# Kernel tuning notes

Hardware: AMD Instinct MI355X
Metric: run time of the kernel (lower is better)

## Reference

```python
import jax, jax.numpy as jnp
import numpy as np


def _segsum(v, idx, n):
    return jax.ops.segment_sum(v, idx, num_segments=n)


def _rdl(z, n_dst, Wna, We, Wi, es, ed, is_, id_):
    """Relationship_Decoupled_layer: node softmax attn + per-edge attn.
    e-channel (mode etype): softmax over 2 logits; i-channel: sigmoid(1 logit)."""
    zd = z[:n_dst]
    node_alpha = jax.nn.softmax(zd @ Wna, axis=1)                      # [nd,2]
    e_e = jax.nn.softmax(jnp.concatenate([z[es], zd[ed]], axis=-1) @ We, axis=1)  # [Ee,2]
    e_i = jax.nn.sigmoid(jnp.concatenate([z[is_], zd[id_]], axis=-1) @ Wi)        # [Ei,1]
    return node_alpha, e_e, e_i


def _one_agg(z, n_dst, W, b, na, e_e, es, ed):
    """One_Neighbor_Aggregation: mean over nbrs of e[:,0]*Linear(z_src), relu, + alpha0*z_dst.
    Linear is applied on src nodes once (linearity) instead of per-edge."""
    zd = na[:, 0:1] * z[:n_dst]
    wz = z @ W + b                                                     # [n_src,D]
    s = _segsum(e_e[:, 0:1] * wz[es], ed, n_dst)                       # [nd,D]
    deg = _segsum(jnp.ones((es.shape[0], 1), z.dtype), ed, n_dst)
    f = jax.nn.relu(s / jnp.maximum(deg, 1.0))
    return f + zd


def _nia(z, n_dst, na, e_e, es, ed, e_i, is_, id_):
    """Neighbor_Interaction_Aggregation: e_h (mode etype, attn col 1) and i_h
    (other etype, sigmoid attn), cross term via polarization identity, + alpha1*z_dst."""
    zd = na[:, 1:2] * z[:n_dst]
    e_h = _segsum(e_e[:, 1:2] * z[es], ed, n_dst)
    i_h = _segsum(e_i * z[is_], id_, n_dst)
    inter = jax.nn.relu(0.5 * (jnp.square(e_h + i_h) - jnp.square(e_h) - jnp.square(i_h)))
    return inter + zd


def setup_inputs() -> dict:
    key = jax.random.key(0)
    ks = jax.random.split(key, 32)
    F, D, O = 256, 128, 64
    n_src0, n_dst0, E0 = 100000, 25000, 500000
    n_src1, n_dst1, E1 = 25000, 5000, 100000

    def ri(k, n, hi):
        return jax.random.randint(k, (n,), 0, hi, dtype=jnp.int32)

    inp = {
        'feat': jax.random.normal(ks[0], (n_src0, F), jnp.float32),
        'src0_cor': ri(ks[1], E0, n_src0), 'dst0_cor': ri(ks[2], E0, n_dst0),
        'src0_sim': ri(ks[3], E0, n_src0), 'dst0_sim': ri(ks[4], E0, n_dst0),
        'src1_cor': ri(ks[5], E1, n_src1), 'dst1_cor': ri(ks[6], E1, n_dst1),
        'src1_sim': ri(ks[7], E1, n_src1), 'dst1_sim': ri(ks[8], E1, n_dst1),
        'n_dst0': n_dst0, 'n_dst1': n_dst1,
    }
    s = 0.05  # keep attention logits / activations in a sane range
    inp['Win'] = jax.random.normal(ks[9], (2, F, D)) * s
    inp['b_in'] = jnp.zeros((2, D), jnp.float32)
    inp['na1'] = jax.random.normal(ks[10], (2, D, 2)) * s
    inp['ea1'] = jax.random.normal(ks[11], (2, 2 * D, 2)) * s
    inp['ia1'] = jax.random.normal(ks[12], (2, 2 * D, 1)) * s
    inp['W1'] = jax.random.normal(ks[13], (2, D, D)) * s
    inp['b1'] = jnp.zeros((2, D), jnp.float32)
    inp['na2'] = jax.random.normal(ks[14], (2, D, 2)) * s
    inp['ea2'] = jax.random.normal(ks[15], (2, 2 * D, 2)) * s
    inp['ia2'] = jax.random.normal(ks[16], (2, 2 * D, 1)) * s
    inp['W2'] = jax.random.normal(ks[17], (2, D, D)) * s
    inp['b2'] = jnp.zeros((2, D), jnp.float32)
    inp['Wout'] = jax.random.normal(ks[18], (2, D, O)) * s
    inp['bout'] = jnp.zeros((2, O), jnp.float32)
    return inp


def reference(feat, src0_cor, dst0_cor, src0_sim, dst0_sim,
              src1_cor, dst1_cor, src1_sim, dst1_sim, n_dst0, n_dst1,
              Win, b_in, na1, ea1, ia1, W1, b1, na2, ea2, ia2, W2, b2, Wout, bout):
    # mode index 0 = 'cor', 1 = 'sim'; e-channel = mode etype, i-channel = other etype
    blk0 = {0: (src0_cor, dst0_cor, src0_sim, dst0_sim),
            1: (src0_sim, dst0_sim, src0_cor, dst0_cor)}
    blk1 = {0: (src1_cor, dst1_cor, src1_sim, dst1_sim),
            1: (src1_sim, dst1_sim, src1_cor, dst1_cor)}
    outs = []
    for m in range(2):
        es0, ed0, is0, id0 = blk0[m]
        es1, ed1, is1, id1 = blk1[m]
        z = feat @ Win[m] + b_in[m]                                    # fc_input (eval: dropout = identity)
        # layer 1 on block0
        na, ee, ei = _rdl(z, n_dst0, na1[m], ea1[m], ia1[m], es0, ed0, is0, id0)
        one = _one_agg(z, n_dst0, W1[m], b1[m], na, ee, es0, ed0)
        nia = _nia(z, n_dst0, na, ee, es0, ed0, ei, is0, id0)
        z = 0.5 * (one + nia)                                          # [n_dst0, D]
        # layer 2 on block1
        na, ee, ei = _rdl(z, n_dst1, na2[m], ea2[m], ia2[m], es1, ed1, is1, id1)
        one = _one_agg(z, n_dst1, W2[m], b2[m], na, ee, es1, ed1)
        nia = _nia(z, n_dst1, na, ee, es1, ed1, ei, is1, id1)
        z = 0.5 * (one + nia)                                          # [n_dst1, D]
        outs.append(z @ Wout[m] + bout[m])
    return jnp.stack(outs)                                             # [2, n_dst1, O] (cor, sim)
```

## Files before the change

### kernel.cpp

```cpp
#include <hip/hip_runtime.h>
#include <hip/hip_bf16.h>
#include <math.h>

#define F_DIM 256
#define D_DIM 128
#define O_DIM 64
#define NS0   100000
#define ND0   25000
#define E0_N  500000
#define NS1   25000
#define ND1   5000
#define E1_N  100000

#define NBE0  1954
#define NBE1  391
#define NB_CSR (2 * NBE0 + 2 * NBE1)
#define NB_WPREP 576

typedef __attribute__((ext_vector_type(8))) short s8v;
typedef __attribute__((ext_vector_type(4))) float f4v;

struct CPtr4 { const int *p0, *p1, *p2, *p3; };
struct MPtr4 { int *p0, *p1, *p2, *p3; };

// ... 138 lines not shown
    else           { wm0 = wave * WM;        wn0 = 0; }

    f4v acc[TM][TN];
    #pragma unroll
    for (int i = 0; i < TM; ++i)
        #pragma unroll
        for (int j = 0; j < TN; ++j)
            acc[i][j] = (f4v)(0.0f);

    for (int kc = 0; kc < KD; kc += 32) {
        __syncthreads();
        #pragma unroll
        for (int it = 0; it < 2; ++it) {
            int f = tid + it * 256;
            int r = f >> 2, g = (f & 3) * 8;
            int gr = row0 + r;
            float4 v = make_float4(0.f, 0.f, 0.f, 0.f);
            if (gr < M) v = *(const float4*)(A + (size_t)gr * KD + kc + g);
            *(float4*)(&As[r * PA + g]) = v;
        }
        #pragma unroll
        for (int it = 0; it < NW * 32 / (256 * 8); ++it) {
            int f = tid + it * 256;
            int r = f >> 2, g = (f & 3) * 8;
            *(float4*)(&Bs[r * PA + g]) = *(const float4*)(Bt + (size_t)r * KD + kc + g);
        }
        __syncthreads();

        s8v af[TM], bfr[TN];
        #pragma unroll
        for (int i = 0; i < TM; ++i)
            af[i] = *(const s8v*)(&As[(wm0 + i * 16 + l15) * PA + l4 * 8]);
        #pragma unroll
        for (int j = 0; j < TN; ++j)
            bfr[j] = *(const s8v*)(&Bs[(wn0 + j * 16 + l15) * PA + l4 * 8]);
        #pragma unroll
        for (int i = 0; i < TM; ++i)
            #pragma unroll
            for (int j = 0; j < TN; ++j)
                acc[i][j] = __builtin_amdgcn_mfma_f32_16x16x32_bf16(
                    af[i], bfr[j], acc[i][j], 0, 0, 0);
    }

    #pragma unroll
    for (int i = 0; i < TM; ++i) {
        #pragma unroll
        for (int ii = 0; ii < 4; ++ii) {
            int row = row0 + wm0 + i * 16 + l4 * 4 + ii;
            if (row < M) {
                #pragma unroll
                for (int j = 0; j < TN; ++j) {
                    int col = wn0 + j * 16 + l15;
                    float a = acc[i][j][ii];
                    if (EPI == 1) {
                        ((float*)Cout)[(size_t)row * NW + col] = a + bias[col];
                    } else {
                        float val = a + cvec[row] * bias[col];
                        float o = partial[(size_t)row * NW + col] + 0.5f * fmaxf(val, 0.f);
                        ((ushort*)Cout)[(size_t)row * NW + col] = f2bf(o);
                    }
                }
            }
        }
    }
}

__global__ void histo4_prep(CPtr4 ed, MPtr4 cnt,
    const float* __restrict__ Win, const float* __restrict__ W1,
    const float* __restrict__ W2,  const float* __restrict__ Wout,
    ushort* __restrict__ Wtin, ushort* __restrict__ Wt1,
    ushort* __restrict__ Wt2,  ushort* __restrict__ Wtout)
{
    int b = blockIdx.x, t = threadIdx.x;
    if (b >= NB_CSR) {
        int i = (b - NB_CSR) * 256 + t;
        if (i < 65536) {
            int m = i >> 15, r = i & 32767, k = r >> 7, n = r & 127;
            Wtin[m * 32768 + n * 256 + k] = f2bf(Win[m * 32768 + k * 128 + n]);
        } else if (i < 98304) {
            int i2 = i - 65536;
            int m = i2 >> 14, r = i2 & 16383, k = r >> 7, n = r & 127;
            Wt1[m * 16384 + n * 128 + k] = f2bf(W1[m * 16384 + k * 128 + n]);
        } else if (i < 131072) {
            int i2 = i - 98304;
            int m = i2 >> 14, r = i2 & 16383, k = r >> 7, n = r & 127;
            Wt2[m * 16384 + n * 128 + k] = f2bf(W2[m * 16384 + k * 128 + n]);
        } else if (i < 147456) {
            int i2 = i - 131072;
            int m = i2 >> 13, r = i2 & 8191, k = r >> 6, n = r & 63;
            Wtout[m * 8192 + n * 128 + k] = f2bf(Wout[m * 8192 + k * 64 + n]);
        }
        return;
    }
    const int* edp; int* cp; int e, E;
    if (b < NBE0)          { edp = ed.p0; cp = cnt.p0; e = b * 256 + t;              E = E0_N; }
    else if (b < 2 * NBE0) { edp = ed.p1; cp = cnt.p1; e = (b - NBE0) * 256 + t;     E = E0_N; }
    else if (b < 2 * NBE0 + NBE1)
                           { edp = ed.p2; cp = cnt.p2; e = (b - 2 * NBE0) * 256 + t; E = E1_N; }
    else                   { edp = ed.p3; cp = cnt.p3; e = (b - 2 * NBE0 - NBE1) * 256 + t; E = E1_N; }
    if (e < E) atomicAdd(&cp[edp[e]], 1);
}

__global__ __launch_bounds__(1024) void exscan4(MPtr4 cnt, MPtr4 row, MPtr4 head)
{
    __shared__ int part[1024];
    const int b = blockIdx.x, t = threadIdx.x;
    int* cp; int* rp; int* hp; int n;
    if (b == 0)      { cp = cnt.p0; rp = row.p0; hp = head.p0; n = ND0; }
    else if (b == 1) { cp = cnt.p1; rp = row.p1; hp = head.p1; n = ND0; }
    else if (b == 2) { cp = cnt.p2; rp = row.p2; hp = head.p2; n = ND1; }
    else             { cp = cnt.p3; rp = row.p3; hp = head.p3; n = ND1; }

    const int chunk = (n + 1023) >> 10;
    const int start = t * chunk;
    int s = 0;
    for (int i = 0; i < chunk; ++i) {
        int idx = start + i;
        if (idx < n) s += cp[idx];
    }
    part[t] = s;
    __syncthreads();
    for (int off = 1; off < 1024; off <<= 1) {
        int v = (t >= off) ? part[t - off] : 0;
        __syncthreads();
        part[t] += v;
        __syncthreads();
    }
    int run = (t == 0) ? 0 : part[t - 1];
    for (int i = 0; i < chunk; ++i) {
        int idx = start + i;
        if (idx < n) { rp[idx] = run; hp[idx] = run; run += cp[idx]; }
    }
    if (t == 1023) rp[n] = part[1023];
}

__global__ void build4(CPtr4 es, CPtr4 ed, MPtr4 head, MPtr4 src)
{
    int b = blockIdx.x, t = threadIdx.x;
    const int *esp, *edp; int *hp, *sp; int e, E;
    if (b < NBE0)          { esp = es.p0; edp = ed.p0; hp = head.p0; sp = src.p0; e = b * 256 + t;              E = E0_N; }
    else if (b < 2 * NBE0) { esp = es.p1; edp = ed.p1; hp = head.p1; sp = src.p1; e = (b - NBE0) * 256 + t;     E = E0_N; }
    else if (b < 2 * NBE0 + NBE1)
                           { esp = es.p2; edp = ed.p2; hp = head.p2; sp = src.p2; e = (b - 2 * NBE0) * 256 + t; E = E1_N; }
    else                   { esp = es.p3; edp = ed.p3; hp = head.p3; sp = src.p3; e = (b - 2 * NBE0 - NBE1) * 256 + t; E = E1_N; }
    if (e >= E) return;
    int p = atomicAdd(&hp[edp[e]], 1);
    sp[p] = esp[e];
}

#define NP_NPB 128
__global__ __launch_bounds__(256) void node_proj(
    const ushort* __restrict__ zb, size_t zstr,
    const float* __restrict__ Web, const float* __restrict__ Wib,
    float* __restrict__ psb, float* __restrict__ qsb,
    float* __restrict__ pdb, float* __restrict__ qdb,
    int n_src, int n_dst)
{
    const int m = blockIdx.y;
    const ushort* z = zb + m * zstr;
    const float* We = Web + m * 512;
    const float* Wi = Wib + m * 256;
    float* ps = psb + (size_t)m * NS0 * 2;
    float* qs = qsb + (size_t)m * NS0;
    float* pd = pdb + (size_t)m * ND0 * 2;
    float* qd = qdb + (size_t)m * ND0;

    __shared__ float w[6][D_DIM];
    for (int k = threadIdx.x; k < D_DIM; k += 256) {
        w[0][k] = We[k * 2 + 0];
        w[1][k] = We[k * 2 + 1];
        w[2][k] = Wi[k];
        w[3][k] = We[(D_DIM + k) * 2 + 0];
        w[4][k] = We[(D_DIM + k) * 2 + 1];
        w[5][k] = Wi[D_DIM + k];
    }
    __syncthreads();

    const int sub = threadIdx.x & 7;
    const int g   = threadIdx.x >> 3;

    float wr[6][16];
    #pragma unroll
    for (int c = 0; c < 6; ++c)
        #pragma unroll
        for (int q = 0; q < 4; ++q) {
            float4 f = *(const float4*)(&w[c][sub * 16 + q * 4]);
            wr[c][q * 4 + 0] = f.x; wr[c][q * 4 + 1] = f.y;
            wr[c][q * 4 + 2] = f.z; wr[c][q * 4 + 3] = f.w;
        }

    #pragma unroll
    for (int it = 0; it < 4; ++it) {
        int node = blockIdx.x * NP_NPB + it * 32 + g;
        if (node >= n_src) continue;
        const ushort* zp = z + (size_t)node * D_DIM + sub * 16;
        uint4 ra = *(const uint4*)zp;
        uint4 rb = *(const uint4*)(zp + 8);
        uint rr[8] = {ra.x, ra.y, ra.z, ra.w, rb.x, rb.y, rb.z, rb.w};
        float p[6] = {0.f, 0.f, 0.f, 0.f, 0.f, 0.f};
        #pragma unroll
        for (int e = 0; e < 8; ++e) {
            float2 f2 = unpack2(rr[e]);
            #pragma unroll
            for (int c = 0; c < 6; ++c)
                p[c] += f2.x * wr[c][2 * e] + f2.y * wr[c][2 * e + 1];
        }
        #pragma unroll
        for (int off = 4; off > 0; off >>= 1)
            #pragma unroll
            for (int c = 0; c < 6; ++c)
                p[c] += __shfl_down(p[c], off);

        if (sub == 0) {
            *(float2*)(ps + (size_t)node * 2) = make_float2(p[0], p[1]);
            qs[node] = p[2];
            if (node < n_dst) {
                *(float2*)(pd + (size_t)node * 2) = make_float2(p[3], p[4]);
                qd[node] = p[5];
            }
        }
    }
}

__global__ __launch_bounds__(256) void edge_gather(
    const ushort* __restrict__ zb, size_t zstr,
    const float* __restrict__ psb, const float* __restrict__ pdb,
    const float* __restrict__ qsb, const float* __restrict__ qdb,
    const int* __restrict__ row_c, const int* __restrict__ src_c,
    const int* __restrict__ row_s, const int* __restrict__ src_s,
    ushort* __restrict__ h0base, float* __restrict__ partialb,
    float* __restrict__ cvecb, int n_dst)
{
    __shared__ uint2 sc[4][64];

    const int m = blockIdx.y;
    const int wv = threadIdx.x >> 6;
    const int d = blockIdx.x * 4 + wv;
    const int lane = threadIdx.x & 63;
    if (d >= n_dst) return;

    const ushort* z = zb + m * zstr;
    const float* ps = psb + (size_t)m * NS0 * 2;
    const float* qs = qsb + (size_t)m * NS0;
    const float* pdv = pdb + (size_t)m * ND0 * 2;
    const float* qdv = qdb + (size_t)m * ND0;
    const int* erow = m ? row_s : row_c;
    const int* esrc = m ? src_s : src_c;
    const int* irow = m ? row_c : row_s;
    const int* isrc = m ? src_c : src_s;
    ushort* h0b = h0base + (size_t)m * ND0 * D_DIM;
    float* partial = partialb + (size_t)m * ND0 * D_DIM;
    float* cvec = cvecb + (size_t)m * ND0;

    const float pd0 = pdv[2 * d], pd1 = pdv[2 * d + 1];
    const float qdd = qdv[d];

    float h0x = 0.f, h0y = 0.f, szx = 0.f, szy = 0.f;
    float ihx = 0.f, ihy = 0.f;
    float se0 = 0.f;

    const int b0 = erow[d], b1 = erow[d + 1];
    for (int base = b0; base < b1; base += 64) {
        const int cnt = min(64, b1 - base);
        if (lane < cnt) {
            int s = esrc[base + lane];
            float2 pp = *(const float2*)(ps + 2 * (size_t)s);
            float l0 = pp.x + pd0, l1 = pp.y + pd1;
            float mx = fmaxf(l0, l1);
            float x0 = __expf(l0 - mx), x1 = __expf(l1 - mx);
            float e0 = x0 / (x0 + x1);
            sc[wv][lane] = make_uint2(f2u(e0), (uint)s);
            se0 += e0;
        }
        asm volatile("s_waitcnt lgkmcnt(0)" ::: "memory");
        const int kf = cnt & ~7;
        int k = 0;
        for (; k < kf; k += 8) {
            uint2 ew[8]; uint rr[8];
            #pragma unroll
            for (int t = 0; t < 8; ++t) ew[t] = sc[wv][k + t];
            #pragma unroll
            for (int t = 0; t < 8; ++t) rr[t] = *(const uint*)(z + (size_t)ew[t].y * D_DIM + lane * 2);
            #pragma unroll
            for (int t = 0; t < 8; ++t) {
                float w0 = u2f(ew[t].x);
                float2 v = unpack2(rr[t]);
                szx += v.x; szy += v.y;
                h0x += w0 * v.x; h0y += w0 * v.y;
            }
        }
        if (k < cnt) {
            uint2 ew[8]; uint rr[8];
            #pragma unroll
            for (int t = 0; t < 8; ++t) ew[t] = sc[wv][(k + t) & 63];
            #pragma unroll
            for (int t = 0; t < 8; ++t) {
                uint s = (k + t < cnt) ? ew[t].y : 0u;
                rr[t] = *(const uint*)(z + (size_t)s * D_DIM + lane * 2);
            }
            #pragma unroll
            for (int t = 0; t < 8; ++t) {
                float sel = (k + t < cnt) ? 1.0f : 0.0f;
                float w0 = u2f(ew[t].x) * sel;
                float2 v = unpack2(rr[t]);
                szx += v.x * sel; szy += v.y * sel;
                h0x += w0 * v.x; h0y += w0 * v.y;
            }
        }
    }

    #pragma unroll
    for (int off = 32; off > 0; off >>= 1)
        se0 += __shfl_down(se0, off);
    if (lane == 0) cvec[d] = se0 / fmaxf((float)(b1 - b0), 1.0f);

    const int c0 = irow[d], c1 = irow[d + 1];
    for (int base = c0; base < c1; base += 64) {
        const int cnt = min(64, c1 - base);
        if (lane < cnt) {
            int s = isrc[base + lane];
            float q = qs[s] + qdd;
            float sg = 1.0f / (1.0f + __expf(-q));
            sc[wv][lane] = make_uint2(f2u(sg), (uint)s);
        }
        asm volatile("s_waitcnt lgkmcnt(0)" ::: "memory");
        const int kf = cnt & ~7;
        int k = 0;
        for (; k < kf; k += 8) {
            uint2 ew[8]; uint rr[8];
            #pragma unroll
            for (int t = 0; t < 8; ++t) ew[t] = sc[wv][k + t];
            #pragma unroll
            for (int t = 0; t < 8; ++t) rr[t] = *(const uint*)(z + (size_t)ew[t].y * D_DIM + lane * 2);
            #pragma unroll
            for (int t = 0; t < 8; ++t) {
                float g = u2f(ew[t].x);
                float2 v = unpack2(rr[t]);
                ihx += g * v.x; ihy += g * v.y;
            }
        }
        if (k < cnt) {
            uint2 ew[8]; uint rr[8];
            #pragma unroll
            for (int t = 0; t < 8; ++t) ew[t] = sc[wv][(k + t) & 63];
            #pragma unroll
            for (int t = 0; t < 8; ++t) {
                uint s = (k + t < cnt) ? ew[t].y : 0u;
                rr[t] = *(const uint*)(z + (size_t)s * D_DIM + lane * 2);
            }
            #pragma unroll
            for (int t = 0; t < 8; ++t) {
                float sel = (k + t < cnt) ? 1.0f : 0.0f;
                float g = u2f(ew[t].x) * sel;
                float2 v = unpack2(rr[t]);
                ihx += g * v.x; ihy += g * v.y;
            }
        }
    }

    float ehx = szx - h0x, ehy = szy - h0y;
    float inv = 1.0f / fmaxf((float)(b1 - b0), 1.0f);
    uint hp = (uint)f2bf(h0x * inv) | ((uint)f2bf(h0y * inv) << 16);
    *(uint*)(h0b + (size_t)d * D_DIM + lane * 2) = hp;

    float2 zd = unpack2(*(const uint*)(z + (size_t)d * D_DIM + lane * 2));
    float px = 0.5f * (fmaxf(ehx * ihx, 0.f) + zd.x);
    float py = 0.5f * (fmaxf(ehy * ihy, 0.f) + zd.y);
    *(float2*)(partial + (size_t)d * D_DIM + lane * 2) = make_float2(px, py);
}

extern "C" void kernel_launch(void* const* d_in, const int* in_sizes, int n_in,
                              void* d_out, int out_size, void* d_ws, size_t ws_size,
                              hipStream_t stream)
{
    const float* feat = (const float*)d_in[0];
    const int* src0_cor = (const int*)d_in[1];
    const int* dst0_cor = (const int*)d_in[2];
    const int* src0_sim = (const int*)d_in[3];
    const int* dst0_sim = (const int*)d_in[4];
    const int* src1_cor = (const int*)d_in[5];
    const int* dst1_cor = (const int*)d_in[6];
    const int* src1_sim = (const int*)d_in[7];
    const int* dst1_sim = (const int*)d_in[8];
    const float* Win  = (const float*)d_in[11];
    const float* b_in = (const float*)d_in[12];
    const float* ea1  = (const float*)d_in[14];
    const float* ia1  = (const float*)d_in[15];
    const float* W1   = (const float*)d_in[16];
    const float* b1   = (const float*)d_in[17];
    const float* ea2  = (const float*)d_in[19];
    const float* ia2  = (const float*)d_in[20];
    const float* W2   = (const float*)d_in[21];
    const float* b2   = (const float*)d_in[22];
    const float* Wout = (const float*)d_in[23];
    const float* bout = (const float*)d_in[24];
    (void)in_sizes; (void)n_in; (void)out_size; (void)ws_size;

    char* wsb = (char*)d_ws;
    size_t off = 0;
    auto alloc_f = [&](size_t n) { float*  p = (float*) (wsb + off); off += n * 4; return p; };
    auto alloc_i = [&](size_t n) { int*    p = (int*)   (wsb + off); off += n * 4; return p; };
    auto alloc_h = [&](size_t n) { ushort* p = (ushort*)(wsb + off); off += ((n * 2 + 15) & ~15ull); return p; };

    ushort* z0b   = alloc_h((size_t)2 * NS0 * D_DIM);
    ushort* z1b   = alloc_h((size_t)2 * NS1 * D_DIM);
    ushort* z2b   = alloc_h((size_t)2 * ND1 * D_DIM);
    ushort* h0b   = alloc_h((size_t)2 * ND0 * D_DIM);
    ushort* Wtin  = alloc_h((size_t)2 * D_DIM * F_DIM);
    ushort* Wt1   = alloc_h((size_t)2 * D_DIM * D_DIM);
    ushort* Wt2   = alloc_h((size_t)2 * D_DIM * D_DIM);
    ushort* Wtout = alloc_h((size_t)2 * O_DIM * D_DIM);

    float* ps      = alloc_f((size_t)2 * NS0 * 2);
    float* qs      = alloc_f((size_t)2 * NS0);
    float* pd      = alloc_f((size_t)2 * ND0 * 2);
    float* qd      = alloc_f((size_t)2 * ND0);
    float* cvec    = alloc_f((size_t)2 * ND0);
    float* partial = alloc_f((size_t)2 * ND0 * D_DIM);

    int* src_c0 = alloc_i(E0_N); int* row_c0 = alloc_i(ND0 + 1);
    int* src_s0 = alloc_i(E0_N); int* row_s0 = alloc_i(ND0 + 1);
    int* src_c1 = alloc_i(E1_N); int* row_c1 = alloc_i(ND1 + 1);
    int* src_s1 = alloc_i(E1_N); int* row_s1 = alloc_i(ND1 + 1);
    int* cnt_all  = alloc_i(2 * ND0 + 2 * ND1);
    int* head_all = alloc_i(2 * ND0 + 2 * ND1);

    int* cnt_c0 = cnt_all;            int* head_c0 = head_all;
    int* cnt_s0 = cnt_all + ND0;      int* head_s0 = head_all + ND0;
    int* cnt_c1 = cnt_all + 2 * ND0;  int* head_c1 = head_all + 2 * ND0;
    int* cnt_s1 = cnt_c1 + ND1;       int* head_s1 = head_c1 + ND1;

    hipMemsetAsync(cnt_all, 0, (size_t)(2 * ND0 + 2 * ND1) * 4, stream);
    {
        CPtr4 edp  = {dst0_cor, dst0_sim, dst1_cor, dst1_sim};
        CPtr4 esp  = {src0_cor, src0_sim, src1_cor, src1_sim};
        MPtr4 cntp = {cnt_c0, cnt_s0, cnt_c1, cnt_s1};
        MPtr4 rowp = {row_c0, row_s0, row_c1, row_s1};
        MPtr4 hdp  = {head_c0, head_s0, head_c1, head_s1};
        MPtr4 srcp = {src_c0, src_s0, src_c1, src_s1};
        histo4_prep<<<NB_CSR + NB_WPREP, 256, 0, stream>>>(
            edp, cntp, Win, W1, W2, Wout, Wtin, Wt1, Wt2, Wtout);
        exscan4<<<4, 1024, 0, stream>>>(cntp, rowp, hdp);
        build4<<<NB_CSR, 256, 0, stream>>>(esp, edp, hdp, srcp);
    }

    const size_t Z0S = (size_t)NS0 * D_DIM, Z1S = (size_t)NS1 * D_DIM;
    const size_t Z2S = (size_t)ND1 * D_DIM, H0S = (size_t)ND0 * D_DIM;

    gemm_l0<<<(NS0 + 63) / 64, 256, 0, stream>>>(
        feat, Wtin, b_in, z0b, Z0S, NS0);

    node_proj<<<dim3((NS0 + NP_NPB - 1) / NP_NPB, 2), 256, 0, stream>>>(
        z0b, Z0S, ea1, ia1, ps, qs, pd, qd, NS0, ND0);
    edge_gather<<<dim3((ND0 + 3) / 4, 2), 256, 0, stream>>>(
        z0b, Z0S, ps, pd, qs, qd, row_c0, src_c0, row_s0, src_s0,
        h0b, partial, cvec, ND0);
    mfma_gemm<128, 128, 2><<<dim3((ND0 + 127) / 128, 2), 256, 0, stream>>>(
        h0b, H0S, Wt1, (size_t)D_DIM * D_DIM, b1, D_DIM,
        cvec, ND0, partial, H0S, z1b, Z1S, ND0);

    node_proj<<<dim3((NS1 + NP_NPB - 1) / NP_NPB, 2), 256, 0, stream>>>(
        z1b, Z1S, ea2, ia2, ps, qs, pd, qd, NS1, ND1);
    edge_gather<<<dim3((ND1 + 3) / 4, 2), 256, 0, stream>>>(
        z1b, Z1S, ps, pd, qs, qd, row_c1, src_c1, row_s1, src_s1,
        h0b, partial, cvec, ND1);
    mfma_gemm<128, 128, 2><<<dim3((ND1 + 127) / 128, 2), 256, 0, stream>>>(
        h0b, H0S, Wt2, (size_t)D_DIM * D_DIM, b2, D_DIM,
        cvec, ND0, partial, H0S, z2b, Z2S, ND1);

    mfma_gemm<64, 128, 1><<<dim3((ND1 + 127) / 128, 2), 256, 0, stream>>>(
        z2b, Z2S, Wtout, (size_t)O_DIM * D_DIM, bout, O_DIM,
        nullptr, 0, nullptr, 0, (float*)d_out, (size_t)ND1 * O_DIM, ND1);
}
```

Before: 549.6 us.

## Merge both modes into one edge-gather pass sharing each edge list

Before, each mode walked the cor and sim edge lists on its own. Now a single kernel walks each edge list once: the two wave halves gather z rows for mode 0 and mode 1 from the same source indices, and both attention weights (softmax and sigmoid) are computed per edge together. The per-node projections are packed into interleaved float4 records (ecor/esim) so one load serves both modes. This halves the index and CSR traffic and removes the separate launch per mode. In exchange, each lane covers 4 features in one mode instead of 2 features across the wave, and half the grid's blocks are gone, so there is less parallelism.

Result: no change. 544.8 us (-0.9%).

```diff
diff --git a/kernel.cpp b/kernel.cpp
--- a/kernel.cpp
+++ b/kernel.cpp
@@ -314,7 +314,7 @@
 __global__ __launch_bounds__(256) void node_proj(
     const ushort* __restrict__ zb, size_t zstr,
     const float* __restrict__ Web, const float* __restrict__ Wib,
-    float* __restrict__ psb, float* __restrict__ qsb,
+    float4* __restrict__ ecor, float4* __restrict__ esim,
     float* __restrict__ pdb, float* __restrict__ qdb,
     int n_src, int n_dst)
 {
@@ -322,10 +322,6 @@
     const ushort* z = zb + m * zstr;
     const float* We = Web + m * 512;
     const float* Wi = Wib + m * 256;
-    float* ps = psb + (size_t)m * NS0 * 2;
-    float* qs = qsb + (size_t)m * NS0;
-    float* pd = pdb + (size_t)m * ND0 * 2;
-    float* qd = qdb + (size_t)m * ND0;
 
     __shared__ float w[6][D_DIM];
     for (int k = threadIdx.x; k < D_DIM; k += 256) {
@@ -374,161 +370,203 @@
                 p[c] += __shfl_down(p[c], off);
 
         if (sub == 0) {
-            *(float2*)(ps + (size_t)node * 2) = make_float2(p[0], p[1]);
-            qs[node] = p[2];
+            if (m == 0) {
+                *(float2*)&ecor[node] = make_float2(p[0], p[1]);
+                ((float*)&esim[node])[2] = p[2];
+            } else {
+                *(float2*)&esim[node] = make_float2(p[0], p[1]);
+                ((float*)&ecor[node])[2] = p[2];
+            }
             if (node < n_dst) {
-                *(float2*)(pd + (size_t)node * 2) = make_float2(p[3], p[4]);
-                qd[node] = p[5];
-            }
-        }
-    }
-}
-
-__global__ __launch_bounds__(256) void edge_gather(
+                *(float2*)(pdb + (size_t)m * ND0 * 2 + 2 * (size_t)node) = make_float2(p[3], p[4]);
+                qdb[(size_t)m * ND0 + node] = p[5];
+            }
+        }
+    }
+}
+
+__global__ __launch_bounds__(256) void edge_gather2(
     const ushort* __restrict__ zb, size_t zstr,
-    const float* __restrict__ psb, const float* __restrict__ pdb,
-    const float* __restrict__ qsb, const float* __restrict__ qdb,
+    const float4* __restrict__ ecor, const float4* __restrict__ esim,
+    const float* __restrict__ pdb, const float* __restrict__ qdb,
     const int* __restrict__ row_c, const int* __restrict__ src_c,
     const int* __restrict__ row_s, const int* __restrict__ src_s,
     ushort* __restrict__ h0base, float* __restrict__ partialb,
     float* __restrict__ cvecb, int n_dst)
 {
-    __shared__ uint2 sc[4][64];
-
-    const int m = blockIdx.y;
+    __shared__ uint4 sc[4][64];
+
     const int wv = threadIdx.x >> 6;
     const int d = blockIdx.x * 4 + wv;
     const int lane = threadIdx.x & 63;
     if (d >= n_dst) return;
 
-    const ushort* z = zb + m * zstr;
-    const float* ps = psb + (size_t)m * NS0 * 2;
-    const float* qs = qsb + (size_t)m * NS0;
-    const float* pdv = pdb + (size_t)m * ND0 * 2;
-    const float* qdv = qdb + (size_t)m * ND0;
-    const int* erow = m ? row_s : row_c;
-    const int* esrc = m ? src_s : src_c;
-    const int* irow = m ? row_c : row_s;
-    const int* isrc = m ? src_c : src_s;
-    ushort* h0b = h0base + (size_t)m * ND0 * D_DIM;
-    float* partial = partialb + (size_t)m * ND0 * D_DIM;
-    float* cvec = cvecb + (size_t)m * ND0;
-
-    const float pd0 = pdv[2 * d], pd1 = pdv[2 * d + 1];
-    const float qdd = qdv[d];
-
-    float h0x = 0.f, h0y = 0.f, szx = 0.f, szy = 0.f;
-    float ihx = 0.f, ihy = 0.f;
-    float se0 = 0.f;
-
-    const int b0 = erow[d], b1 = erow[d + 1];
+    const int half = lane >> 5;
+    const int sub  = lane & 31;
+    const ushort* zlane = zb + (size_t)half * zstr + sub * 4;
+
+    const float pc0 = pdb[2 * d], pc1 = pdb[2 * d + 1];
+    const float pm0 = pdb[2 * ND0 + 2 * d], pm1 = pdb[2 * ND0 + 2 * d + 1];
+    const float qd0 = qdb[d], qd1 = qdb[ND0 + d];
+
+    float aH1[4] = {0,0,0,0}, aS1[4] = {0,0,0,0};
+    float aH2[4] = {0,0,0,0}, aS2[4] = {0,0,0,0};
+    float sec = 0.f, ses = 0.f;
+
+    const int b0 = row_c[d], b1 = row_c[d + 1];
+    const int c0 = row_s[d], c1 = row_s[d + 1];
+
     for (int base = b0; base < b1; base += 64) {
         const int cnt = min(64, b1 - base);
         if (lane < cnt) {
-            int s = esrc[base + lane];
-            float2 pp = *(const float2*)(ps + 2 * (size_t)s);
-            float l0 = pp.x + pd0, l1 = pp.y + pd1;
+            int s = src_c[base + lane];
+            float4 t = ecor[s];
+            float l0 = t.x + pc0, l1 = t.y + pc1;
             float mx = fmaxf(l0, l1);
             float x0 = __expf(l0 - mx), x1 = __expf(l1 - mx);
             float e0 = x0 / (x0 + x1);
-            sc[wv][lane] = make_uint2(f2u(e0), (uint)s);
-            se0 += e0;
+            float sg = 1.0f / (1.0f + __expf(-(t.z + qd1)));
+            sc[wv][lane] = make_uint4(f2u(e0), f2u(sg), (uint)s, 0u);
+            sec += e0;
         }
         asm volatile("s_waitcnt lgkmcnt(0)" ::: "memory");
-        const int kf = cnt & ~7;
-        int k = 0;
+        int k = 0; const int kf = cnt & ~7;
         for (; k < kf; k += 8) {
-            uint2 ew[8]; uint rr[8];
-            #pragma unroll
-            for (int t = 0; t < 8; ++t) ew[t] = sc[wv][k + t];
-            #pragma unroll
-            for (int t = 0; t < 8; ++t) rr[t] = *(const uint*)(z + (size_t)ew[t].y * D_DIM + lane * 2);
-            #pragma unroll
-            for (int t = 0; t < 8; ++t) {
-                float w0 = u2f(ew[t].x);
-                float2 v = unpack2(rr[t]);
-                szx += v.x; szy += v.y;
-                h0x += w0 * v.x; h0y += w0 * v.y;
+            float w8[8]; uint s8[8]; uint2 rr[8];
+            #pragma unroll
+            for (int t2 = 0; t2 < 8; ++t2) {
+                uint4 e4 = sc[wv][k + t2];
+                w8[t2] = u2f(half ? e4.y : e4.x); s8[t2] = e4.z;
+            }
+            #pragma unroll
+            for (int t2 = 0; t2 < 8; ++t2)
+                rr[t2] = *(const uint2*)(zlane + (size_t)s8[t2] * D_DIM);
+            #pragma unroll
+            for (int t2 = 0; t2 < 8; ++t2) {
+                float2 v0 = unpack2(rr[t2].x), v1 = unpack2(rr[t2].y);
+                float w = w8[t2];
+                aS1[0] += v0.x;     aS1[1] += v0.y;     aS1[2] += v1.x;     aS1[3] += v1.y;
+                aH1[0] += w * v0.x; aH1[1] += w * v0.y; aH1[2] += w * v1.x; aH1[3] += w * v1.y;
             }
         }
         if (k < cnt) {
-            uint2 ew[8]; uint rr[8];
-            #pragma unroll
-            for (int t = 0; t < 8; ++t) ew[t] = sc[wv][(k + t) & 63];
-            #pragma unroll
-            for (int t = 0; t < 8; ++t) {
-                uint s = (k + t < cnt) ? ew[t].y : 0u;
-                rr[t] = *(const uint*)(z + (size_t)s * D_DIM + lane * 2);
-            }
-            #pragma unroll
-            for (int t = 0; t < 8; ++t) {
-                float sel = (k + t < cnt) ? 1.0f : 0.0f;
-                float w0 = u2f(ew[t].x) * sel;
-                float2 v = unpack2(rr[t]);
-                szx += v.x * sel; szy += v.y * sel;
-                h0x += w0 * v.x; h0y += w0 * v.y;
-            }
-        }
-    }
-
-    #pragma unroll
-    for (int off = 32; off > 0; off >>= 1)
-        se0 += __shfl_down(se0, off);
-    if (lane == 0) cvec[d] = se0 / fmaxf((float)(b1 - b0), 1.0f);
-
-    const int c0 = irow[d], c1 = irow[d + 1];
+            float w8[8], m8[8]; uint s8[8]; uint2 rr[8];
+            #pragma unroll
+            for (int t2 = 0; t2 < 8; ++t2) {
+                uint4 e4 = sc[wv][(k + t2) & 63];
+                bool ok = (k + t2 < cnt);
+                m8[t2] = ok ? 1.0f : 0.0f;
+                w8[t2] = ok ? u2f(half ? e4.y : e4.x) : 0.0f;
+                s8[t2] = ok ? e4.z : 0u;
+            }
+            #pragma unroll
+            for (int t2 = 0; t2 < 8; ++t2)
+                rr[t2] = *(const uint2*)(zlane + (size_t)s8[t2] * D_DIM);
+            #pragma unroll
+            for (int t2 = 0; t2 < 8; ++t2) {
+                float2 v0 = unpack2(rr[t2].x), v1 = unpack2(rr[t2].y);
+                float w = w8[t2], mm = m8[t2];
+                aS1[0] += mm * v0.x; aS1[1] += mm * v0.y; aS1[2] += mm * v1.x; aS1[3] += mm * v1.y;
+                aH1[0] += w * v0.x;  aH1[1] += w * v0.y;  aH1[2] += w * v1.x;  aH1[3] += w * v1.y;
+            }
+        }
+    }
+
     for (int base = c0; base < c1; base += 64) {
         const int cnt = min(64, c1 - base);
         if (lane < cnt) {
-            int s = isrc[base + lane];
-            float q = qs[s] + qdd;
-            float sg = 1.0f / (1.0f + __expf(-q));
-            sc[wv][lane] = make_uint2(f2u(sg), (uint)s);
+            int s = src_s[base + lane];
+            float4 t = esim[s];
+            float l0 = t.x + pm0, l1 = t.y + pm1;
+            float mx = fmaxf(l0, l1);
+            float x0 = __expf(l0 - mx), x1 = __expf(l1 - mx);
+            float e0 = x0 / (x0 + x1);
+            float sg = 1.0f / (1.0f + __expf(-(t.z + qd0)));
+            sc[wv][lane] = make_uint4(f2u(sg), f2u(e0), (uint)s, 0u);
+            ses += e0;
         }
         asm volatile("s_waitcnt lgkmcnt(0)" ::: "memory");
-        const int kf = cnt & ~7;
-        int k = 0;
+        int k = 0; const int kf = cnt & ~7;
         for (; k < kf; k += 8) {
-            uint2 ew[8]; uint rr[8];
-            #pragma unroll
-            for (int t = 0; t < 8; ++t) ew[t] = sc[wv][k + t];
-            #pragma unroll
-            for (int t = 0; t < 8; ++t) rr[t] = *(const uint*)(z + (size_t)ew[t].y * D_DIM + lane * 2);
-            #pragma unroll
-            for (int t = 0; t < 8; ++t) {
-                float g = u2f(ew[t].x);
-                float2 v = unpack2(rr[t]);
-                ihx += g * v.x; ihy += g * v.y;
+            float w8[8]; uint s8[8]; uint2 rr[8];
+            #pragma unroll
+            for (int t2 = 0; t2 < 8; ++t2) {
+                uint4 e4 = sc[wv][k + t2];
+                w8[t2] = u2f(half ? e4.y : e4.x); s8[t2] = e4.z;
+            }
+            #pragma unroll
+            for (int t2 = 0; t2 < 8; ++t2)
+                rr[t2] = *(const uint2*)(zlane + (size_t)s8[t2] * D_DIM);
+            #pragma unroll
+            for (int t2 = 0; t2 < 8; ++t2) {
+                float2 v0 = unpack2(rr[t2].x), v1 = unpack2(rr[t2].y);
+                float w = w8[t2];
+                aS2[0] += v0.x;     aS2[1] += v0.y;     aS2[2] += v1.x;     aS2[3] += v1.y;
+                aH2[0] += w * v0.x; aH2[1] += w * v0.y; aH2[2] += w * v1.x; aH2[3] += w * v1.y;
             }
         }
         if (k < cnt) {
-            uint2 ew[8]; uint rr[8];
-            #pragma unroll
-            for (int t = 0; t < 8; ++t) ew[t] = sc[wv][(k + t) & 63];
-            #pragma unroll
-            for (int t = 0; t < 8; ++t) {
-                uint s = (k + t < cnt) ? ew[t].y : 0u;
-                rr[t] = *(const uint*)(z + (size_t)s * D_DIM + lane * 2);
-            }
-            #pragma unroll
-            for (int t = 0; t < 8; ++t) {
-                float sel = (k + t < cnt) ? 1.0f : 0.0f;
-                float g = u2f(ew[t].x) * sel;
-                float2 v = unpack2(rr[t]);
-                ihx += g * v.x; ihy += g * v.y;
-            }
-        }
-    }
-
-    float ehx = szx - h0x, ehy = szy - h0y;
-    float inv = 1.0f / fmaxf((float)(b1 - b0), 1.0f);
-    uint hp = (uint)f2bf(h0x * inv) | ((uint)f2bf(h0y * inv) << 16);
-    *(uint*)(h0b + (size_t)d * D_DIM + lane * 2) = hp;
-
-    float2 zd = unpack2(*(const uint*)(z + (size_t)d * D_DIM + lane * 2));
-    float px = 0.5f * (fmaxf(ehx * ihx, 0.f) + zd.x);
-    float py = 0.5f * (fmaxf(ehy * ihy, 0.f) + zd.y);
-    *(float2*)(partial + (size_t)d * D_DIM + lane * 2) = make_float2(px, py);
+            float w8[8], m8[8]; uint s8[8]; uint2 rr[8];
+            #pragma unroll
+            for (int t2 = 0; t2 < 8; ++t2) {
+                uint4 e4 = sc[wv][(k + t2) & 63];
+                bool ok = (k + t2 < cnt);
+                m8[t2] = ok ? 1.0f : 0.0f;
+                w8[t2] = ok ? u2f(half ? e4.y : e4.x) : 0.0f;
+                s8[t2] = ok ? e4.z : 0u;
+            }
+            #pragma unroll
+            for (int t2 = 0; t2 < 8; ++t2)
+                rr[t2] = *(const uint2*)(zlane + (size_t)s8[t2] * D_DIM);
+            #pragma unroll
+            for (int t2 = 0; t2 < 8; ++t2) {
+                float2 v0 = unpack2(rr[t2].x), v1 = unpack2(rr[t2].y);
+                float w = w8[t2], mm = m8[t2];
+                aS2[0] += mm * v0.x; aS2[1] += mm * v0.y; aS2[2] += mm * v1.x; aS2[3] += mm * v1.y;
+                aH2[0] += w * v0.x;  aH2[1] += w * v0.y;  aH2[2] += w * v1.x;  aH2[3] += w * v1.y;
+            }
+        }
+    }
+
+    #pragma unroll
+    for (int off = 32; off > 0; off >>= 1) {
+        sec += __shfl_down(sec, off);
+        ses += __shfl_down(ses, off);
+    }
+    const int degc = b1 - b0, degs = c1 - c0;
+    if (lane == 0) {
+        cvecb[d]       = sec / fmaxf((float)degc, 1.0f);
+        cvecb[ND0 + d] = ses / fmaxf((float)degs, 1.0f);
+    }
+
+    float h0r[4], szr[4], ihr[4];
+    #pragma unroll
+    for (int j2 = 0; j2 < 4; ++j2) {
+        h0r[j2] = half ? aH2[j2] : aH1[j2];
+        szr[j2] = half ? aS2[j2] : aS1[j2];
+        ihr[j2] = half ? aH1[j2] : aH2[j2];
+    }
+    const int deg = half ? degs : degc;
+    const float inv = 1.0f / fmaxf((float)deg, 1.0f);
+
+    uint2 zr = *(const uint2*)(zlane + (size_t)d * D_DIM);
+    float2 zlo = unpack2(zr.x), zhi = unpack2(zr.y);
+    float zd4[4] = {zlo.x, zlo.y, zhi.x, zhi.y};
+
+    float pt[4]; ushort hb[4];
+    #pragma unroll
+    for (int j2 = 0; j2 < 4; ++j2) {
+        float eh = szr[j2] - h0r[j2];
+        pt[j2] = 0.5f * (fmaxf(eh * ihr[j2], 0.0f) + zd4[j2]);
+        hb[j2] = f2bf(h0r[j2] * inv);
+    }
+    uint hp0 = (uint)hb[0] | ((uint)hb[1] << 16);
+    uint hp1 = (uint)hb[2] | ((uint)hb[3] << 16);
+    const size_t MSTR = (size_t)ND0 * D_DIM;
+    *(uint2*)(h0base + (size_t)half * MSTR + (size_t)d * D_DIM + sub * 4) =
+        make_uint2(hp0, hp1);
+    *(float4*)(partialb + (size_t)half * MSTR + (size_t)d * D_DIM + sub * 4) =
+        make_float4(pt[0], pt[1], pt[2], pt[3]);
 }
 
 extern "C" void kernel_launch(void* const* d_in, const int* in_sizes, int n_in,
@@ -560,9 +598,10 @@
 
     char* wsb = (char*)d_ws;
     size_t off = 0;
-    auto alloc_f = [&](size_t n) { float*  p = (float*) (wsb + off); off += n * 4; return p; };
-    auto alloc_i = [&](size_t n) { int*    p = (int*)   (wsb + off); off += n * 4; return p; };
-    auto alloc_h = [&](size_t n) { ushort* p = (ushort*)(wsb + off); off += ((n * 2 + 15) & ~15ull); return p; };
+    auto alloc_f  = [&](size_t n) { float*  p = (float*) (wsb + off); off += n * 4; return p; };
+    auto alloc_f4 = [&](size_t n) { float4* p = (float4*)(wsb + off); off += n * 16; return p; };
+    auto alloc_i  = [&](size_t n) { int*    p = (int*)   (wsb + off); off += n * 4; return p; };
+    auto alloc_h  = [&](size_t n) { ushort* p = (ushort*)(wsb + off); off += ((n * 2 + 15) & ~15ull); return p; };
 
     ushort* z0b   = alloc_h((size_t)2 * NS0 * D_DIM);
     ushort* z1b   = alloc_h((size_t)2 * NS1 * D_DIM);
@@ -573,8 +612,8 @@
     ushort* Wt2   = alloc_h((size_t)2 * D_DIM * D_DIM);
     ushort* Wtout = alloc_h((size_t)2 * O_DIM * D_DIM);
 
-    float* ps      = alloc_f((size_t)2 * NS0 * 2);
-    float* qs      = alloc_f((size_t)2 * NS0);
+    float4* ecor   = alloc_f4((size_t)NS0);
+    float4* esim   = alloc_f4((size_t)NS0);
     float* pd      = alloc_f((size_t)2 * ND0 * 2);
     float* qd      = alloc_f((size_t)2 * ND0);
     float* cvec    = alloc_f((size_t)2 * ND0);
@@ -613,18 +652,18 @@
         feat, Wtin, b_in, z0b, Z0S, NS0);
 
     node_proj<<<dim3((NS0 + NP_NPB - 1) / NP_NPB, 2), 256, 0, stream>>>(
-        z0b, Z0S, ea1, ia1, ps, qs, pd, qd, NS0, ND0);
-    edge_gather<<<dim3((ND0 + 3) / 4, 2), 256, 0, stream>>>(
-        z0b, Z0S, ps, pd, qs, qd, row_c0, src_c0, row_s0, src_s0,
+        z0b, Z0S, ea1, ia1, ecor, esim, pd, qd, NS0, ND0);
+    edge_gather2<<<(ND0 + 3) / 4, 256, 0, stream>>>(
+        z0b, Z0S, ecor, esim, pd, qd, row_c0, src_c0, row_s0, src_s0,
         h0b, partial, cvec, ND0);
     mfma_gemm<128, 128, 2><<<dim3((ND0 + 127) / 128, 2), 256, 0, stream>>>(
         h0b, H0S, Wt1, (size_t)D_DIM * D_DIM, b1, D_DIM,
         cvec, ND0, partial, H0S, z1b, Z1S, ND0);
 
     node_proj<<<dim3((NS1 + NP_NPB - 1) / NP_NPB, 2), 256, 0, stream>>>(
-        z1b, Z1S, ea2, ia2, ps, qs, pd, qd, NS1, ND1);
-    edge_gather<<<dim3((ND1 + 3) / 4, 2), 256, 0, stream>>>(
-        z1b, Z1S, ps, pd, qs, qd, row_c1, src_c1, row_s1, src_s1,
+        z1b, Z1S, ea2, ia2, ecor, esim, pd, qd, NS1, ND1);
+    edge_gather2<<<(ND1 + 3) / 4, 256, 0, stream>>>(
+        z1b, Z1S, ecor, esim, pd, qd, row_c1, src_c1, row_s1, src_s1,
         h0b, partial, cvec, ND1);
     mfma_gemm<128, 128, 2><<<dim3((ND1 + 127) / 128, 2), 256, 0, stream>>>(
         h0b, H0S, Wt2, (size_t)D_DIM * D_DIM, b2, D_DIM,
```

## Interleave e- and i-channel neighbor gathers and pack per-source logits by edge type

Applied to the files above, without the earlier changes.

The edge gather kernel now runs the e-channel and i-channel neighbor loops together when both degree lists fit in one 64-wide chunk. This puts the bf16 row loads for both channels in flight at once instead of running two serial dependent loops, and keeps a general fallback path for larger degrees. Node projection results are reorganized into two float4 tables indexed by edge type, so each edge's logit lookup comes from one table keyed by its source node. The interleaved loop runs to the larger of the two degrees, which costs extra masked loads when the two degrees differ a lot.

Result: no change. 555.1 us (+1.0%).

```diff
diff --git a/kernel.cpp b/kernel.cpp
--- a/kernel.cpp
+++ b/kernel.cpp
@@ -314,7 +314,7 @@
 __global__ __launch_bounds__(256) void node_proj(
     const ushort* __restrict__ zb, size_t zstr,
     const float* __restrict__ Web, const float* __restrict__ Wib,
-    float* __restrict__ psb, float* __restrict__ qsb,
+    float4* __restrict__ ecor, float4* __restrict__ esim,
     float* __restrict__ pdb, float* __restrict__ qdb,
     int n_src, int n_dst)
 {
@@ -322,10 +322,6 @@
     const ushort* z = zb + m * zstr;
     const float* We = Web + m * 512;
     const float* Wi = Wib + m * 256;
-    float* ps = psb + (size_t)m * NS0 * 2;
-    float* qs = qsb + (size_t)m * NS0;
-    float* pd = pdb + (size_t)m * ND0 * 2;
-    float* qd = qdb + (size_t)m * ND0;
 
     __shared__ float w[6][D_DIM];
     for (int k = threadIdx.x; k < D_DIM; k += 256) {
@@ -374,26 +370,32 @@
                 p[c] += __shfl_down(p[c], off);
 
         if (sub == 0) {
-            *(float2*)(ps + (size_t)node * 2) = make_float2(p[0], p[1]);
-            qs[node] = p[2];
+            if (m == 0) {
+                *(float2*)&ecor[node] = make_float2(p[0], p[1]);
+                ((float*)&esim[node])[2] = p[2];
+            } else {
+                *(float2*)&esim[node] = make_float2(p[0], p[1]);
+                ((float*)&ecor[node])[2] = p[2];
+            }
             if (node < n_dst) {
-                *(float2*)(pd + (size_t)node * 2) = make_float2(p[3], p[4]);
-                qd[node] = p[5];
-            }
-        }
-    }
-}
-
-__global__ __launch_bounds__(256) void edge_gather(
+                *(float2*)(pdb + (size_t)m * ND0 * 2 + 2 * (size_t)node) = make_float2(p[3], p[4]);
+                qdb[(size_t)m * ND0 + node] = p[5];
+            }
+        }
+    }
+}
+
+__global__ __launch_bounds__(256) void edge_gather3(
     const ushort* __restrict__ zb, size_t zstr,
-    const float* __restrict__ psb, const float* __restrict__ pdb,
-    const float* __restrict__ qsb, const float* __restrict__ qdb,
+    const float4* __restrict__ ecor, const float4* __restrict__ esim,
+    const float* __restrict__ pdb, const float* __restrict__ qdb,
     const int* __restrict__ row_c, const int* __restrict__ src_c,
     const int* __restrict__ row_s, const int* __restrict__ src_s,
     ushort* __restrict__ h0base, float* __restrict__ partialb,
     float* __restrict__ cvecb, int n_dst)
 {
-    __shared__ uint2 sc[4][64];
+    __shared__ uint2 scE[4][64];
+    __shared__ uint2 scI[4][64];
 
     const int m = blockIdx.y;
     const int wv = threadIdx.x >> 6;
@@ -401,72 +403,137 @@
     const int lane = threadIdx.x & 63;
     if (d >= n_dst) return;
 
-    const ushort* z = zb + m * zstr;
-    const float* ps = psb + (size_t)m * NS0 * 2;
-    const float* qs = qsb + (size_t)m * NS0;
-    const float* pdv = pdb + (size_t)m * ND0 * 2;
-    const float* qdv = qdb + (size_t)m * ND0;
+    const ushort* z = zb + (size_t)m * zstr;
+    const ushort* zlane = z + lane * 2;
+
     const int* erow = m ? row_s : row_c;
     const int* esrc = m ? src_s : src_c;
     const int* irow = m ? row_c : row_s;
     const int* isrc = m ? src_c : src_s;
-    ushort* h0b = h0base + (size_t)m * ND0 * D_DIM;
-    float* partial = partialb + (size_t)m * ND0 * D_DIM;
-    float* cvec = cvecb + (size_t)m * ND0;
-
-    const float pd0 = pdv[2 * d], pd1 = pdv[2 * d + 1];
-    const float qdd = qdv[d];
+    const float4* etab = m ? esim : ecor;
+    const float4* itab = m ? ecor : esim;
+
+    const float pd0 = pdb[(size_t)m * ND0 * 2 + 2 * d];
+    const float pd1 = pdb[(size_t)m * ND0 * 2 + 2 * d + 1];
+    const float qdd = qdb[(size_t)m * ND0 + d];
 
     float h0x = 0.f, h0y = 0.f, szx = 0.f, szy = 0.f;
     float ihx = 0.f, ihy = 0.f;
     float se0 = 0.f;
 
     const int b0 = erow[d], b1 = erow[d + 1];
-    for (int base = b0; base < b1; base += 64) {
-        const int cnt = min(64, b1 - base);
-        if (lane < cnt) {
-            int s = esrc[base + lane];
-            float2 pp = *(const float2*)(ps + 2 * (size_t)s);
-            float l0 = pp.x + pd0, l1 = pp.y + pd1;
+    const int c0 = irow[d], c1 = irow[d + 1];
+    const int nE = b1 - b0, nI = c1 - c0;
+
+    if (nE <= 64 && nI <= 64) {
+        const bool aE = lane < nE, aI = lane < nI;
+        int sE = 0, sI = 0;
+        if (aE) sE = esrc[b0 + lane];
+        if (aI) sI = isrc[c0 + lane];
+        float2 tE = make_float2(0.f, 0.f);
+        float  tI = 0.f;
+        if (aE) tE = *(const float2*)&etab[sE];
+        if (aI) tI = ((const float*)&itab[sI])[2];
+        if (aE) {
+            float l0 = tE.x + pd0, l1 = tE.y + pd1;
             float mx = fmaxf(l0, l1);
             float x0 = __expf(l0 - mx), x1 = __expf(l1 - mx);
             float e0 = x0 / (x0 + x1);
-            sc[wv][lane] = make_uint2(f2u(e0), (uint)s);
-            se0 += e0;
+            scE[wv][lane] = make_uint2(f2u(e0), (uint)sE);
+            se0 = e0;
+        }
+        if (aI) {
+            float sg = 1.0f / (1.0f + __expf(-(tI + qdd)));
+            scI[wv][lane] = make_uint2(f2u(sg), (uint)sI);
         }
         asm volatile("s_waitcnt lgkmcnt(0)" ::: "memory");
-        const int kf = cnt & ~7;
-        int k = 0;
-        for (; k < kf; k += 8) {
-            uint2 ew[8]; uint rr[8];
-            #pragma unroll
-            for (int t = 0; t < 8; ++t) ew[t] = sc[wv][k + t];
-            #pragma unroll
-            for (int t = 0; t < 8; ++t) rr[t] = *(const uint*)(z + (size_t)ew[t].y * D_DIM + lane * 2);
+
+        const int kmax = (nE > nI) ? nE : nI;
+        for (int k = 0; k < kmax; k += 8) {
+            float wE[8], mE[8], wI[8];
+            uint rE[8], rI[8];
             #pragma unroll
             for (int t = 0; t < 8; ++t) {
-                float w0 = u2f(ew[t].x);
-                float2 v = unpack2(rr[t]);
-                szx += v.x; szy += v.y;
-                h0x += w0 * v.x; h0y += w0 * v.y;
-            }
-        }
-        if (k < cnt) {
-            uint2 ew[8]; uint rr[8];
-            #pragma unroll
-            for (int t = 0; t < 8; ++t) ew[t] = sc[wv][(k + t) & 63];
+                uint2 e2 = scE[wv][(k + t) & 63];
+                bool ok = (k + t < nE);
+                mE[t] = ok ? 1.0f : 0.0f;
+                wE[t] = ok ? u2f(e2.x) : 0.0f;
+                rE[t] = *(const uint*)(zlane + (size_t)(ok ? e2.y : 0u) * D_DIM);
+            }
             #pragma unroll
             for (int t = 0; t < 8; ++t) {
-                uint s = (k + t < cnt) ? ew[t].y : 0u;
-                rr[t] = *(const uint*)(z + (size_t)s * D_DIM + lane * 2);
+                uint2 e2 = scI[wv][(k + t) & 63];
+                bool ok = (k + t < nI);
+                wI[t] = ok ? u2f(e2.x) : 0.0f;
+                rI[t] = *(const uint*)(zlane + (size_t)(ok ? e2.y : 0u) * D_DIM);
             }
             #pragma unroll
             for (int t = 0; t < 8; ++t) {
-                float sel = (k + t < cnt) ? 1.0f : 0.0f;
-                float w0 = u2f(ew[t].x) * sel;
-                float2 v = unpack2(rr[t]);
-                szx += v.x * sel; szy += v.y * sel;
-                h0x += w0 * v.x; h0y += w0 * v.y;
+                float2 v = unpack2(rE[t]);
+                szx += mE[t] * v.x; szy += mE[t] * v.y;
+                h0x += wE[t] * v.x; h0y += wE[t] * v.y;
+            }
+            #pragma unroll
+            for (int t = 0; t < 8; ++t) {
+                float2 v = unpack2(rI[t]);
+                ihx += wI[t] * v.x; ihy += wI[t] * v.y;
+            }
+        }
+    } else {
+        for (int base = b0; base < b1; base += 64) {
+            const int cnt = min(64, b1 - base);
+            if (lane < cnt) {
+                int s = esrc[base + lane];
+                float2 t = *(const float2*)&etab[s];
+                float l0 = t.x + pd0, l1 = t.y + pd1;
+                float mx = fmaxf(l0, l1);
+                float x0 = __expf(l0 - mx), x1 = __expf(l1 - mx);
+                float e0 = x0 / (x0 + x1);
+                scE[wv][lane] = make_uint2(f2u(e0), (uint)s);
+                se0 += e0;
+            }
+            asm volatile("s_waitcnt lgkmcnt(0)" ::: "memory");
+            for (int k = 0; k < cnt; k += 8) {
+                float w8[8], m8[8]; uint rr[8];
+                #pragma unroll
+                for (int t = 0; t < 8; ++t) {
+                    uint2 e2 = scE[wv][(k + t) & 63];
+                    bool ok = (k + t < cnt);
+                    m8[t] = ok ? 1.0f : 0.0f;
+                    w8[t] = ok ? u2f(e2.x) : 0.0f;
+                    rr[t] = *(const uint*)(zlane + (size_t)(ok ? e2.y : 0u) * D_DIM);
+                }
+                #pragma unroll
+                for (int t = 0; t < 8; ++t) {
+                    float2 v = unpack2(rr[t]);
+                    szx += m8[t] * v.x; szy += m8[t] * v.y;
+                    h0x += w8[t] * v.x; h0y += w8[t] * v.y;
+                }
+            }
+        }
+        for (int base = c0; base < c1; base += 64) {
+            const int cnt = min(64, c1 - base);
+            if (lane < cnt) {
+                int s = isrc[base + lane];
+                float ti = ((const float*)&itab[s])[2];
+                float sg = 1.0f / (1.0f + __expf(-(ti + qdd)));
+                scI[wv][lane] = make_uint2(f2u(sg), (uint)s);
+            }
+            asm volatile("s_waitcnt lgkmcnt(0)" ::: "memory");
+            for (int k = 0; k < cnt; k += 8) {
+                float w8[8]; uint rr[8];
+                #pragma unroll
+                for (int t = 0; t < 8; ++t) {
+                    uint2 e2 = scI[wv][(k + t) & 63];
+                    bool ok = (k + t < cnt);
+                    w8[t] = ok ? u2f(e2.x) : 0.0f;
+                    rr[t] = *(const uint*)(zlane + (size_t)(ok ? e2.y : 0u) * D_DIM);
+                }
+                #pragma unroll
+                for (int t = 0; t < 8; ++t) {
+                    float2 v = unpack2(rr[t]);
+                    ihx += w8[t] * v.x; ihy += w8[t] * v.y;
+                }
             }
         }
     }
@@ -474,61 +541,20 @@
     #pragma unroll
     for (int off = 32; off > 0; off >>= 1)
         se0 += __shfl_down(se0, off);
-    if (lane == 0) cvec[d] = se0 / fmaxf((float)(b1 - b0), 1.0f);
-
-    const int c0 = irow[d], c1 = irow[d + 1];
-    for (int base = c0; base < c1; base += 64) {
-        const int cnt = min(64, c1 - base);
-        if (lane < cnt) {
-            int s = isrc[base + lane];
-            float q = qs[s] + qdd;
-            float sg = 1.0f / (1.0f + __expf(-q));
-            sc[wv][lane] = make_uint2(f2u(sg), (uint)s);
-        }
-        asm volatile("s_waitcnt lgkmcnt(0)" ::: "memory");
-        const int kf = cnt & ~7;
-        int k = 0;
-        for (; k < kf; k += 8) {
-            uint2 ew[8]; uint rr[8];
-            #pragma unroll
-            for (int t = 0; t < 8; ++t) ew[t] = sc[wv][k + t];
-            #pragma unroll
-            for (int t = 0; t < 8; ++t) rr[t] = *(const uint*)(z + (size_t)ew[t].y * D_DIM + lane * 2);
-            #pragma unroll
-            for (int t = 0; t < 8; ++t) {
-                float g = u2f(ew[t].x);
-                float2 v = unpack2(rr[t]);
-                ihx += g * v.x; ihy += g * v.y;
-            }
-        }
-        if (k < cnt) {
-            uint2 ew[8]; uint rr[8];
-            #pragma unroll
-            for (int t = 0; t < 8; ++t) ew[t] = sc[wv][(k + t) & 63];
-            #pragma unroll
-            for (int t = 0; t < 8; ++t) {
-                uint s = (k + t < cnt) ? ew[t].y : 0u;
-                rr[t] = *(const uint*)(z + (size_t)s * D_DIM + lane * 2);
-            }
-            #pragma unroll
-            for (int t = 0; t < 8; ++t) {
-                float sel = (k + t < cnt) ? 1.0f : 0.0f;
-                float g = u2f(ew[t].x) * sel;
-                float2 v = unpack2(rr[t]);
-                ihx += g * v.x; ihy += g * v.y;
-            }
-        }
-    }
+    if (lane == 0)
+        cvecb[(size_t)m * ND0 + d] = se0 / fmaxf((float)nE, 1.0f);
 
     float ehx = szx - h0x, ehy = szy - h0y;
-    float inv = 1.0f / fmaxf((float)(b1 - b0), 1.0f);
+    float inv = 1.0f / fmaxf((float)nE, 1.0f);
     uint hp = (uint)f2bf(h0x * inv) | ((uint)f2bf(h0y * inv) << 16);
-    *(uint*)(h0b + (size_t)d * D_DIM + lane * 2) = hp;
-
-    float2 zd = unpack2(*(const uint*)(z + (size_t)d * D_DIM + lane * 2));
+    const size_t MSTR = (size_t)ND0 * D_DIM;
+    *(uint*)(h0base + (size_t)m * MSTR + (size_t)d * D_DIM + lane * 2) = hp;
+
+    float2 zd = unpack2(*(const uint*)(zlane + (size_t)d * D_DIM));
     float px = 0.5f * (fmaxf(ehx * ihx, 0.f) + zd.x);
     float py = 0.5f * (fmaxf(ehy * ihy, 0.f) + zd.y);
-    *(float2*)(partial + (size_t)d * D_DIM + lane * 2) = make_float2(px, py);
+    *(float2*)(partialb + (size_t)m * MSTR + (size_t)d * D_DIM + lane * 2) =
+        make_float2(px, py);
 }
 
 extern "C" void kernel_launch(void* const* d_in, const int* in_sizes, int n_in,
@@ -560,9 +586,10 @@
 
     char* wsb = (char*)d_ws;
     size_t off = 0;
-    auto alloc_f = [&](size_t n) { float*  p = (float*) (wsb + off); off += n * 4; return p; };
-    auto alloc_i = [&](size_t n) { int*    p = (int*)   (wsb + off); off += n * 4; return p; };
-    auto alloc_h = [&](size_t n) { ushort* p = (ushort*)(wsb + off); off += ((n * 2 + 15) & ~15ull); return p; };
+    auto alloc_f  = [&](size_t n) { float*  p = (float*) (wsb + off); off += n * 4; return p; };
+    auto alloc_f4 = [&](size_t n) { float4* p = (float4*)(wsb + off); off += n * 16; return p; };
+    auto alloc_i  = [&](size_t n) { int*    p = (int*)   (wsb + off); off += n * 4; return p; };
+    auto alloc_h  = [&](size_t n) { ushort* p = (ushort*)(wsb + off); off += ((n * 2 + 15) & ~15ull); return p; };
 
     ushort* z0b   = alloc_h((size_t)2 * NS0 * D_DIM);
     ushort* z1b   = alloc_h((size_t)2 * NS1 * D_DIM);
@@ -573,8 +600,8 @@
     ushort* Wt2   = alloc_h((size_t)2 * D_DIM * D_DIM);
     ushort* Wtout = alloc_h((size_t)2 * O_DIM * D_DIM);
 
-    float* ps      = alloc_f((size_t)2 * NS0 * 2);
-    float* qs      = alloc_f((size_t)2 * NS0);
+    float4* ecor   = alloc_f4((size_t)NS0);
+    float4* esim   = alloc_f4((size_t)NS0);
     float* pd      = alloc_f((size_t)2 * ND0 * 2);
     float* qd      = alloc_f((size_t)2 * ND0);
     float* cvec    = alloc_f((size_t)2 * ND0);
@@ -613,18 +640,18 @@
         feat, Wtin, b_in, z0b, Z0S, NS0);
 
     node_proj<<<dim3((NS0 + NP_NPB - 1) / NP_NPB, 2), 256, 0, stream>>>(
-        z0b, Z0S, ea1, ia1, ps, qs, pd, qd, NS0, ND0);
-    edge_gather<<<dim3((ND0 + 3) / 4, 2), 256, 0, stream>>>(
-        z0b, Z0S, ps, pd, qs, qd, row_c0, src_c0, row_s0, src_s0,
+        z0b, Z0S, ea1, ia1, ecor, esim, pd, qd, NS0, ND0);
+    edge_gather3<<<dim3((ND0 + 3) / 4, 2), 256, 0, stream>>>(
+        z0b, Z0S, ecor, esim, pd, qd, row_c0, src_c0, row_s0, src_s0,
         h0b, partial, cvec, ND0);
     mfma_gemm<128, 128, 2><<<dim3((ND0 + 127) / 128, 2), 256, 0, stream>>>(
         h0b, H0S, Wt1, (size_t)D_DIM * D_DIM, b1, D_DIM,
         cvec, ND0, partial, H0S, z1b, Z1S, ND0);
 
     node_proj<<<dim3((NS1 + NP_NPB - 1) / NP_NPB, 2), 256, 0, stream>>>(
-        z1b, Z1S, ea2, ia2, ps, qs, pd, qd, NS1, ND1);
-    edge_gather<<<dim3((ND1 + 3) / 4, 2), 256, 0, stream>>>(
-        z1b, Z1S, ps, pd, qs, qd, row_c1, src_c1, row_s1, src_s1,
+        z1b, Z1S, ea2, ia2, ecor, esim, pd, qd, NS1, ND1);
+    edge_gather3<<<dim3((ND1 + 3) / 4, 2), 256, 0, stream>>>(
+        z1b, Z1S, ecor, esim, pd, qd, row_c1, src_c1, row_s1, src_s1,
         h0b, partial, cvec, ND1);
     mfma_gemm<128, 128, 2><<<dim3((ND1 + 127) / 128, 2), 256, 0, stream>>>(
         h0b, H0S, Wt2, (size_t)D_DIM * D_DIM, b2, D_DIM,
```
